# Optimization experiments

Measured on AMD Instinct MI355X. Metric: run time of the kernel, lower is better.

Reference implementation:

```python
import jax, jax.numpy as jnp
import numpy as np

SEQ, D_IN, D_OUT = 8192, 1024, 1024


def setup_inputs() -> dict:
    key = jax.random.key(0)
    kx, kq, kk, kv = jax.random.split(key, 4)
    # torch nn.Linear weights have shape (out_features, in_features)
    s = 1.0 / np.sqrt(D_IN)
    return {
        "x": jax.random.normal(kx, (SEQ, D_IN), dtype=jnp.float32),
        "Wq": jax.random.uniform(kq, (D_OUT, D_IN), dtype=jnp.float32, minval=-s, maxval=s),
        "Wk": jax.random.uniform(kk, (D_OUT, D_IN), dtype=jnp.float32, minval=-s, maxval=s),
        "Wv": jax.random.uniform(kv, (D_OUT, D_IN), dtype=jnp.float32, minval=-s, maxval=s),
    }


def reference(x, Wq, Wk, Wv):
    # Linear (no bias): y = x @ W.T
    q = x @ Wq.T          # [S, D_OUT]
    k = x @ Wk.T          # [S, D_OUT]
    v = x @ Wv.T          # [S, D_OUT]
    scale = 1.0 / jnp.sqrt(jnp.asarray(k.shape[-1], dtype=x.dtype))
    scores = (q @ k.T) * scale            # [S, S]
    weights = jax.nn.softmax(scores, axis=-1)
    return weights @ v                    # [S, D_OUT]
```

## Files before the change

kernel.cpp:

```cpp
#include <hip/hip_runtime.h>
#include <hip/hip_bf16.h>
#include <stdint.h>


#define SEQ 8192
#define DMODEL 1024
#define LOG2E 1.44269504088896340736f
#define GROUP_M 8

typedef __bf16 bf16_t;
typedef __bf16 bf16x8 __attribute__((ext_vector_type(8)));
typedef float f32x4 __attribute__((ext_vector_type(4)));

__global__ __launch_bounds__(256)
void convert_f32_bf16(const float* __restrict__ in, bf16_t* __restrict__ out, long n) {
    long i = ((long)blockIdx.x * 256 + threadIdx.x) * 4;
    if (i + 3 < n) {
        const float4 v = *(const float4*)(in + i);
        union { ushort4 u; bf16_t b[4]; } p;
        p.b[0] = (bf16_t)v.x; p.b[1] = (bf16_t)v.y;
        p.b[2] = (bf16_t)v.z; p.b[3] = (bf16_t)v.w;
        *(ushort4*)(out + i) = p.u;
    }
}

__global__ __launch_bounds__(256)
void add_f32(float* __restrict__ out, const float* __restrict__ part, long n) {
    long i = ((long)blockIdx.x * 256 + threadIdx.x) * 4;
    if (i + 3 < n) {
        float4 a = *(const float4*)(out + i);
        const float4 b = *(const float4*)(part + i);
        a.x += b.x; a.y += b.y; a.z += b.z; a.w += b.w;
        *(float4*)(out + i) = a;
    }
}

__global__ __launch_bounds__(256)
void zero_f32(float* __restrict__ p, int n) {
    int i = blockIdx.x * 256 + threadIdx.x;
    if (i < n) p[i] = 0.0f;
}

template <typename OutT, int MODE>
__global__ __launch_bounds__(512, 2)
void gemm_nt(const bf16_t* __restrict__ A, const bf16_t* __restrict__ B,
             OutT* __restrict__ C0, OutT* __restrict__ C1,
             float* __restrict__ lsum,
             int M, int N, int Kps, int lda, int ldb, int ldc,
             long plane, int cshift, float alpha)
{
    __shared__ bf16_t As[2][256 * 64];
    __shared__ bf16_t Bs[2][256 * 64];

    const int tid  = threadIdx.x;
    const int wave = tid >> 6;
    const int lane = tid & 63;

    const int nbm = M >> 8, nbn = N >> 8;
    const int tiles = nbm * nbn;
    int bid = blockIdx.x;
    const int sid = bid / tiles;
    bid -= sid * tiles;
    const long kbase = (long)sid * Kps;
    OutT* __restrict__ C = sid ? C1 : C0;

    const int per_group = GROUP_M * nbn;
    const int gid   = bid / per_group;
    const int rem   = bid - gid * per_group;
    const int first = gid * GROUP_M;
    const int gsz   = min(nbm - first, GROUP_M);
    const int bm    = first + rem % gsz;
    const int bn    = rem / gsz;
    const long row0 = (long)bm * 256;
    const long col0 = (long)bn * 256;

    const int wm = (wave >> 2) * 128;
    const int wn = (wave & 3) * 64;
    const int lr = lane & 15;
    const int lq = lane >> 4;

    const int rt = tid >> 3;
    const int sl = ((tid & 7) + rt) & 7;
    const bf16_t* pa = A + (row0 + rt) * (long)lda + kbase + sl * 8;
    const bf16_t* pb = B + (col0 + rt) * (long)ldb + kbase + sl * 8;

    const int p0  = (lq - lr) & 7;
    const int p1  = p0 ^ 4;
    const int oA0 = (wm + lr) * 64 + p0 * 8;
    const int oA1 = (wm + lr) * 64 + p1 * 8;
    const int oB0 = (wn + lr) * 64 + p0 * 8;
    const int oB1 = (wn + lr) * 64 + p1 * 8;

    const int nt = Kps >> 6;

    f32x4 acc[8][4] = {};

#define STG8(kt, bsel)                                                          \
    {                                                                           \
        _Pragma("unroll")                                                       \
        for (int i = 0; i < 4; ++i) {                                           \
            const bf16_t* ga = pa + (long)(kt) * 64 + (long)i * 64 * lda;       \
            __builtin_amdgcn_global_load_lds(                                   \
                (const __attribute__((address_space(1))) uint32_t*)ga,          \
                (__attribute__((address_space(3))) uint32_t*)(As[bsel] + i * 4096 + tid * 8), \
                16, 0, 0);                                                      \
        }                                                                       \
        _Pragma("unroll")                                                       \
        for (int i = 0; i < 4; ++i) {                                           \
            const bf16_t* gb = pb + (long)(kt) * 64 + (long)i * 64 * ldb;       \
            __builtin_amdgcn_global_load_lds(                                   \
                (const __attribute__((address_space(1))) uint32_t*)gb,          \
                (__attribute__((address_space(3))) uint32_t*)(Bs[bsel] + i * 4096 + tid * 8), \
                16, 0, 0);                                                      \
        }                                                                       \
    }

    STG8(0, 0);

    for (int t = 0; t < nt; ++t) {
        const int c = t & 1;
        const bf16_t* as = As[c];
        const bf16_t* bs = Bs[c];

        asm volatile("s_waitcnt vmcnt(0)" ::: "memory");
        __builtin_amdgcn_s_barrier();
        asm volatile("" ::: "memory");

        if (t + 1 < nt) STG8(t + 1, c ^ 1);

        bf16x8 a0k0[4], a0k1[4], b0k0[2], b0k1[2], b1k0[2], b1k1[2];
        #pragma unroll
        for (int mi = 0; mi < 4; ++mi) {
            a0k0[mi] = *(const bf16x8*)(as + oA0 + mi * 1024);
            a0k1[mi] = *(const bf16x8*)(as + oA1 + mi * 1024);
        }
        #pragma unroll
        for (int ni = 0; ni < 2; ++ni) {
            b0k0[ni] = *(const bf16x8*)(bs + oB0 + ni * 1024);
            b0k1[ni] = *(const bf16x8*)(bs + oB1 + ni * 1024);
            b1k0[ni] = *(const bf16x8*)(bs + oB0 + (ni + 2) * 1024);
            b1k1[ni] = *(const bf16x8*)(bs + oB1 + (ni + 2) * 1024);
        }

        __builtin_amdgcn_s_setprio(1);
        #pragma unroll
        for (int mi = 0; mi < 4; ++mi)
            #pragma unroll
            for (int ni = 0; ni < 2; ++ni)
                acc[mi][ni] = __builtin_amdgcn_mfma_f32_16x16x32_bf16(
                    a0k0[mi], b0k0[ni], acc[mi][ni], 0, 0, 0);
        #pragma unroll
        for (int mi = 0; mi < 4; ++mi)
            #pragma unroll
            for (int ni = 0; ni < 2; ++ni)
                acc[mi][ni] = __builtin_amdgcn_mfma_f32_16x16x32_bf16(
                    a0k1[mi], b0k1[ni], acc[mi][ni], 0, 0, 0);

        #pragma unroll
        for (int mi = 0; mi < 4; ++mi)
            #pragma unroll
            for (int ni = 0; ni < 2; ++ni)
                acc[mi][ni + 2] = __builtin_amdgcn_mfma_f32_16x16x32_bf16(
                    a0k0[mi], b1k0[ni], acc[mi][ni + 2], 0, 0, 0);
        #pragma unroll
        for (int mi = 0; mi < 4; ++mi)
            #pragma unroll
            for (int ni = 0; ni < 2; ++ni)
                acc[mi][ni + 2] = __builtin_amdgcn_mfma_f32_16x16x32_bf16(
                    a0k1[mi], b1k1[ni], acc[mi][ni + 2], 0, 0, 0);
        __builtin_amdgcn_s_setprio(0);

        bf16x8 a1k0[4], a1k1[4];
        #pragma unroll
        for (int mi = 0; mi < 4; ++mi) {
            a1k0[mi] = *(const bf16x8*)(as + oA0 + (mi + 4) * 1024);
            a1k1[mi] = *(const bf16x8*)(as + oA1 + (mi + 4) * 1024);
        }

        __builtin_amdgcn_s_setprio(1);
        #pragma unroll
        for (int mi = 0; mi < 4; ++mi)
            #pragma unroll
            for (int ni = 0; ni < 2; ++ni)
                acc[mi + 4][ni] = __builtin_amdgcn_mfma_f32_16x16x32_bf16(
                    a1k0[mi], b0k0[ni], acc[mi + 4][ni], 0, 0, 0);
        #pragma unroll
        for (int mi = 0; mi < 4; ++mi)
            #pragma unroll
            for (int ni = 0; ni < 2; ++ni)
                acc[mi + 4][ni] = __builtin_amdgcn_mfma_f32_16x16x32_bf16(
                    a1k1[mi], b0k1[ni], acc[mi + 4][ni], 0, 0, 0);

        #pragma unroll
        for (int mi = 0; mi < 4; ++mi)
            #pragma unroll
            for (int ni = 0; ni < 2; ++ni)
                acc[mi + 4][ni + 2] = __builtin_amdgcn_mfma_f32_16x16x32_bf16(
                    a1k0[mi], b1k0[ni], acc[mi + 4][ni + 2], 0, 0, 0);
        #pragma unroll
        for (int mi = 0; mi < 4; ++mi)
            #pragma unroll
            for (int ni = 0; ni < 2; ++ni)
                acc[mi + 4][ni + 2] = __builtin_amdgcn_mfma_f32_16x16x32_bf16(
                    a1k1[mi], b1k1[ni], acc[mi + 4][ni + 2], 0, 0, 0);
        __builtin_amdgcn_s_setprio(0);
    }
#undef STG8

    OutT* __restrict__ Cb = C + (col0 >> cshift) * plane;
    const int ccol0 = (int)(col0 & (((long)1 << cshift) - 1));

    if (MODE == 1) {
        #pragma unroll
        for (int mi = 0; mi < 8; ++mi)
            #pragma unroll
            for (int rg = 0; rg < 4; ++rg) {
                const long r = row0 + wm + mi * 16 + lq * 4 + rg;
                float part = 0.f;
                #pragma unroll
                for (int ni = 0; ni < 4; ++ni) {
                    const int cc = ccol0 + wn + ni * 16 + lr;
                    const float e = exp2f(alpha * acc[mi][ni][rg]);
                    part += e;
                    Cb[r * (long)ldc + cc] = (OutT)e;
                }
                part += __shfl_xor(part, 1);
                part += __shfl_xor(part, 2);
                part += __shfl_xor(part, 4);
                part += __shfl_xor(part, 8);
                if (lr == 0) atomicAdd(&lsum[r], part);
            }
    } else if (MODE == 2) {
        #pragma unroll
        for (int mi = 0; mi < 8; ++mi)
            #pragma unroll
            for (int rg = 0; rg < 4; ++rg) {
                const long r = row0 + wm + mi * 16 + lq * 4 + rg;
                const float inv = 1.0f / lsum[r];
                #pragma unroll
                for (int ni = 0; ni < 4; ++ni) {
                    const int cc = ccol0 + wn + ni * 16 + lr;
                    Cb[r * (long)ldc + cc] = (OutT)(acc[mi][ni][rg] * inv);
                }
            }
    } else {
        #pragma unroll
        for (int mi = 0; mi < 8; ++mi)
            #pragma unroll
            for (int ni = 0; ni < 4; ++ni)
                #pragma unroll
                for (int rg = 0; rg < 4; ++rg) {
                    const long r = row0 + wm + mi * 16 + lq * 4 + rg;
                    const int  cc = ccol0 + wn + ni * 16 + lr;
                    Cb[r * (long)ldc + cc] = (OutT)(alpha * acc[mi][ni][rg]);
                }
    }
}

__global__ __launch_bounds__(256)
void transpose_bf16(const bf16_t* __restrict__ in, bf16_t* __restrict__ out,
                    int R, int ldin, int ldout)
{
    __shared__ bf16_t tile[32][33];
    const int tx = threadIdx.x & 31;
    const int ty = threadIdx.x >> 5;
    const int c0 = blockIdx.x * 32;
    const int r0 = blockIdx.y * 32;
    #pragma unroll
    for (int j = 0; j < 32; j += 8)
        tile[ty + j][tx] = in[(long)(r0 + ty + j) * ldin + c0 + tx];
    __syncthreads();
    #pragma unroll
    for (int j = 0; j < 32; j += 8)
        out[(long)(c0 + ty + j) * ldout + r0 + tx] = tile[tx][ty + j];
}

extern "C" void kernel_launch(void* const* d_in, const int* in_sizes, int n_in,
                              void* d_out, int out_size, void* d_ws, size_t ws_size,
                              hipStream_t stream)
{
    const float* x  = (const float*)d_in[0];
    const float* Wq = (const float*)d_in[1];
    const float* Wk = (const float*)d_in[2];
    const float* Wv = (const float*)d_in[3];
    float* out = (float*)d_out;

    char* ws = (char*)d_ws;
    const long XN = (long)SEQ * DMODEL;
    const long WN = (long)DMODEL * DMODEL;
    const long SN = (long)SEQ * SEQ;

    bf16_t* xb   = (bf16_t*)ws;
    bf16_t* wcat = (bf16_t*)(ws + XN * 2);
    bf16_t* qb   = (bf16_t*)(ws + XN * 2 + WN * 6);
    bf16_t* kb   = qb + XN;
    bf16_t* vb   = qb + 2 * XN;
    bf16_t* Sb   = (bf16_t*)(ws + XN * 2 + WN * 6 + XN * 6);
    float*  pvp  = (float*)(ws + XN * 2 + WN * 6 + XN * 6 + SN * 2);
    float*  lsum = (float*)(ws + XN * 2 + WN * 6 + XN * 6 + SN * 2 + XN * 4);
    bf16_t* vtb  = xb;

    const size_t base_need = (size_t)(XN * 2 + WN * 6 + XN * 6 + SN * 2);
    const bool use_split = ws_size >= base_need + XN * 4 + SEQ * 4;
    if (!use_split) lsum = (float*)(ws + base_need);

    convert_f32_bf16<<<(int)(XN / 4 / 256), 256, 0, stream>>>(x,  xb, XN);
    convert_f32_bf16<<<(int)(WN / 4 / 256), 256, 0, stream>>>(Wq, wcat,          WN);
    convert_f32_bf16<<<(int)(WN / 4 / 256), 256, 0, stream>>>(Wk, wcat + WN,     WN);
    convert_f32_bf16<<<(int)(WN / 4 / 256), 256, 0, stream>>>(Wv, wcat + 2 * WN, WN);
    zero_f32<<<SEQ / 256, 256, 0, stream>>>(lsum, SEQ);

    dim3 blk256(256);
    dim3 blk512(512);
    gemm_nt<bf16_t, 0><<<(SEQ / 256) * (3 * DMODEL / 256), blk512, 0, stream>>>(
        xb, wcat, qb, qb, nullptr, SEQ, 3 * DMODEL, DMODEL,
        DMODEL, DMODEL, DMODEL, XN, 10, 1.0f);

    transpose_bf16<<<dim3(DMODEL / 32, SEQ / 32), blk256, 0, stream>>>(
        vb, vtb, SEQ, DMODEL, SEQ);

    gemm_nt<bf16_t, 1><<<(SEQ / 256) * (SEQ / 256), blk512, 0, stream>>>(
        qb, kb, Sb, Sb, lsum, SEQ, SEQ, DMODEL,
        DMODEL, DMODEL, SEQ, 0, 30, 0.03125f * LOG2E);

    if (use_split) {
        gemm_nt<float, 2><<<2 * (SEQ / 256) * (DMODEL / 256), blk512, 0, stream>>>(
            Sb, vtb, out, pvp, lsum, SEQ, DMODEL, SEQ / 2,
            SEQ, SEQ, DMODEL, 0, 30, 1.0f);
        add_f32<<<(int)(XN / 4 / 256), 256, 0, stream>>>(out, pvp, XN);
    } else {
        gemm_nt<float, 2><<<(SEQ / 256) * (DMODEL / 256), blk512, 0, stream>>>(
            Sb, vtb, out, out, lsum, SEQ, DMODEL, SEQ,
            SEQ, SEQ, DMODEL, 0, 30, 1.0f);
    }
}
```

Measured before the change: 512.0 us.

## Load B operand directly from global into registers for QKV and QK^T GEMMs

Adds a BDIR template path in which each wave loads its B fragments straight from global memory into registers, double-buffered across k-steps, while only A is staged through LDS. This halves LDS use for those GEMMs (which may allow more blocks per CU) and removes LDS reads for B. The cost is redundant global/L2 traffic, because waves sharing columns each fetch B separately, and higher register pressure. The PV GEMM keeps the original LDS path for both operands.

```diff
diff --git a/kernel.cpp b/kernel.cpp
--- a/kernel.cpp
+++ b/kernel.cpp
@@ -41,7 +41,7 @@
     if (i < n) p[i] = 0.0f;
 }
 
-template <typename OutT, int MODE>
+template <typename OutT, int MODE, int BDIR>
 __global__ __launch_bounds__(512, 2)
 void gemm_nt(const bf16_t* __restrict__ A, const bf16_t* __restrict__ B,
              OutT* __restrict__ C0, OutT* __restrict__ C1,
@@ -49,8 +49,7 @@
              int M, int N, int Kps, int lda, int ldb, int ldc,
              long plane, int cshift, float alpha)
 {
-    __shared__ bf16_t As[2][256 * 64];
-    __shared__ bf16_t Bs[2][256 * 64];
+    __shared__ bf16_t smem[(BDIR ? 2 : 4) * 16384];
 
     const int tid  = threadIdx.x;
     const int wave = tid >> 6;
@@ -95,117 +94,196 @@
 
     f32x4 acc[8][4] = {};
 
-#define STG8(kt, bsel)                                                          \
+#define STG4(kt, base, psrc, ld)                                                \
     {                                                                           \
         _Pragma("unroll")                                                       \
         for (int i = 0; i < 4; ++i) {                                           \
-            const bf16_t* ga = pa + (long)(kt) * 64 + (long)i * 64 * lda;       \
+            const bf16_t* g_ = (psrc) + (long)(kt) * 64 + (long)i * 64 * (ld);  \
             __builtin_amdgcn_global_load_lds(                                   \
-                (const __attribute__((address_space(1))) uint32_t*)ga,          \
-                (__attribute__((address_space(3))) uint32_t*)(As[bsel] + i * 4096 + tid * 8), \
+                (const __attribute__((address_space(1))) uint32_t*)g_,          \
+                (__attribute__((address_space(3))) uint32_t*)((base) + i * 4096 + tid * 8), \
                 16, 0, 0);                                                      \
         }                                                                       \
-        _Pragma("unroll")                                                       \
-        for (int i = 0; i < 4; ++i) {                                           \
-            const bf16_t* gb = pb + (long)(kt) * 64 + (long)i * 64 * ldb;       \
-            __builtin_amdgcn_global_load_lds(                                   \
-                (const __attribute__((address_space(1))) uint32_t*)gb,          \
-                (__attribute__((address_space(3))) uint32_t*)(Bs[bsel] + i * 4096 + tid * 8), \
-                16, 0, 0);                                                      \
-        }                                                                       \
-    }
-
-    STG8(0, 0);
-
-    for (int t = 0; t < nt; ++t) {
-        const int c = t & 1;
-        const bf16_t* as = As[c];
-        const bf16_t* bs = Bs[c];
-
-        asm volatile("s_waitcnt vmcnt(0)" ::: "memory");
-        __builtin_amdgcn_s_barrier();
-        asm volatile("" ::: "memory");
-
-        if (t + 1 < nt) STG8(t + 1, c ^ 1);
-
-        bf16x8 a0k0[4], a0k1[4], b0k0[2], b0k1[2], b1k0[2], b1k1[2];
-        #pragma unroll
-        for (int mi = 0; mi < 4; ++mi) {
-            a0k0[mi] = *(const bf16x8*)(as + oA0 + mi * 1024);
-            a0k1[mi] = *(const bf16x8*)(as + oA1 + mi * 1024);
+    }
+
+    if constexpr (BDIR) {
+        const bf16_t* gB[4];
+        #pragma unroll
+        for (int ni = 0; ni < 4; ++ni)
+            gB[ni] = B + (col0 + wn + ni * 16 + lr) * (long)ldb + kbase + lq * 8;
+
+        bf16x8 bA[8], bB[8];
+
+        #pragma unroll
+        for (int ni = 0; ni < 4; ++ni) {
+            bA[ni * 2 + 0] = *(const bf16x8*)(gB[ni]);
+            bA[ni * 2 + 1] = *(const bf16x8*)(gB[ni] + 32);
         }
-        #pragma unroll
-        for (int ni = 0; ni < 2; ++ni) {
-            b0k0[ni] = *(const bf16x8*)(bs + oB0 + ni * 1024);
-            b0k1[ni] = *(const bf16x8*)(bs + oB1 + ni * 1024);
-            b1k0[ni] = *(const bf16x8*)(bs + oB0 + (ni + 2) * 1024);
-            b1k1[ni] = *(const bf16x8*)(bs + oB1 + (ni + 2) * 1024);
+        STG4(0, smem, pa, lda);
+        #pragma unroll
+        for (int ni = 0; ni < 4; ++ni) gB[ni] += 64;
+
+#define BDIR_BODY(t, BU, BF)                                                    \
+        {                                                                       \
+            const int c_ = (t) & 1;                                             \
+            const bf16_t* as = smem + c_ * 16384;                               \
+                        \
+            asm volatile("s_waitcnt vmcnt(0)" ::: "memory");                    \
+            __builtin_amdgcn_s_barrier();                                       \
+            asm volatile("" ::: "memory");                                      \
+            if ((t) + 1 < nt) {                                                 \
+                _Pragma("unroll")                                               \
+                for (int ni = 0; ni < 4; ++ni) {                                \
+                    BF[ni * 2 + 0] = *(const bf16x8*)(gB[ni]);                  \
+                    BF[ni * 2 + 1] = *(const bf16x8*)(gB[ni] + 32);             \
+                }                                                               \
+                STG4((t) + 1, smem + (c_ ^ 1) * 16384, pa, lda);                \
+            }                                                                   \
+            _Pragma("unroll")                                                   \
+            for (int ni = 0; ni < 4; ++ni) gB[ni] += 64;                        \
+            bf16x8 a0[4], a1[4];                                                \
+            _Pragma("unroll")                                                   \
+            for (int mi = 0; mi < 4; ++mi) {                                    \
+                a0[mi] = *(const bf16x8*)(as + oA0 + mi * 1024);                \
+                a1[mi] = *(const bf16x8*)(as + oA1 + mi * 1024);                \
+            }                                                                   \
+            __builtin_amdgcn_s_setprio(1);                                      \
+            _Pragma("unroll")                                                   \
+            for (int mi = 0; mi < 4; ++mi)                                      \
+                _Pragma("unroll")                                               \
+                for (int ni = 0; ni < 4; ++ni)                                  \
+                    acc[mi][ni] = __builtin_amdgcn_mfma_f32_16x16x32_bf16(      \
+                        a0[mi], BU[ni * 2 + 0], acc[mi][ni], 0, 0, 0);          \
+            _Pragma("unroll")                                                   \
+            for (int mi = 0; mi < 4; ++mi)                                      \
+                _Pragma("unroll")                                               \
+                for (int ni = 0; ni < 4; ++ni)                                  \
+                    acc[mi][ni] = __builtin_amdgcn_mfma_f32_16x16x32_bf16(      \
+                        a1[mi], BU[ni * 2 + 1], acc[mi][ni], 0, 0, 0);          \
+            __builtin_amdgcn_s_setprio(0);                                      \
+            bf16x8 a2[4], a3[4];                                                \
+            _Pragma("unroll")                                                   \
+            for (int mi = 0; mi < 4; ++mi) {                                    \
+                a2[mi] = *(const bf16x8*)(as + oA0 + (mi + 4) * 1024);          \
+                a3[mi] = *(const bf16x8*)(as + oA1 + (mi + 4) * 1024);          \
+            }                                                                   \
+            __builtin_amdgcn_s_setprio(1);                                      \
+            _Pragma("unroll")                                                   \
+            for (int mi = 0; mi < 4; ++mi)                                      \
+                _Pragma("unroll")                                               \
+                for (int ni = 0; ni < 4; ++ni)                                  \
+                    acc[mi + 4][ni] = __builtin_amdgcn_mfma_f32_16x16x32_bf16(  \
+                        a2[mi], BU[ni * 2 + 0], acc[mi + 4][ni], 0, 0, 0);      \
+            _Pragma("unroll")                                                   \
+            for (int mi = 0; mi < 4; ++mi)                                      \
+                _Pragma("unroll")                                               \
+                for (int ni = 0; ni < 4; ++ni)                                  \
+                    acc[mi + 4][ni] = __builtin_amdgcn_mfma_f32_16x16x32_bf16(  \
+                        a3[mi], BU[ni * 2 + 1], acc[mi + 4][ni], 0, 0, 0);      \
+            __builtin_amdgcn_s_setprio(0);                                      \
         }
 
-        __builtin_amdgcn_s_setprio(1);
-        #pragma unroll
-        for (int mi = 0; mi < 4; ++mi)
-            #pragma unroll
-            for (int ni = 0; ni < 2; ++ni)
-                acc[mi][ni] = __builtin_amdgcn_mfma_f32_16x16x32_bf16(
-                    a0k0[mi], b0k0[ni], acc[mi][ni], 0, 0, 0);
-        #pragma unroll
-        for (int mi = 0; mi < 4; ++mi)
-            #pragma unroll
-            for (int ni = 0; ni < 2; ++ni)
-                acc[mi][ni] = __builtin_amdgcn_mfma_f32_16x16x32_bf16(
-                    a0k1[mi], b0k1[ni], acc[mi][ni], 0, 0, 0);
-
-        #pragma unroll
-        for (int mi = 0; mi < 4; ++mi)
-            #pragma unroll
-            for (int ni = 0; ni < 2; ++ni)
-                acc[mi][ni + 2] = __builtin_amdgcn_mfma_f32_16x16x32_bf16(
-                    a0k0[mi], b1k0[ni], acc[mi][ni + 2], 0, 0, 0);
-        #pragma unroll
-        for (int mi = 0; mi < 4; ++mi)
-            #pragma unroll
-            for (int ni = 0; ni < 2; ++ni)
-                acc[mi][ni + 2] = __builtin_amdgcn_mfma_f32_16x16x32_bf16(
-                    a0k1[mi], b1k1[ni], acc[mi][ni + 2], 0, 0, 0);
-        __builtin_amdgcn_s_setprio(0);
-
-        bf16x8 a1k0[4], a1k1[4];
-        #pragma unroll
-        for (int mi = 0; mi < 4; ++mi) {
-            a1k0[mi] = *(const bf16x8*)(as + oA0 + (mi + 4) * 1024);
-            a1k1[mi] = *(const bf16x8*)(as + oA1 + (mi + 4) * 1024);
+        for (int t = 0; t < nt; t += 2) {
+            BDIR_BODY(t,     bA, bB);
+            BDIR_BODY(t + 1, bB, bA);
         }
-
-        __builtin_amdgcn_s_setprio(1);
-        #pragma unroll
-        for (int mi = 0; mi < 4; ++mi)
-            #pragma unroll
-            for (int ni = 0; ni < 2; ++ni)
-                acc[mi + 4][ni] = __builtin_amdgcn_mfma_f32_16x16x32_bf16(
-                    a1k0[mi], b0k0[ni], acc[mi + 4][ni], 0, 0, 0);
-        #pragma unroll
-        for (int mi = 0; mi < 4; ++mi)
-            #pragma unroll
-            for (int ni = 0; ni < 2; ++ni)
-                acc[mi + 4][ni] = __builtin_amdgcn_mfma_f32_16x16x32_bf16(
-                    a1k1[mi], b0k1[ni], acc[mi + 4][ni], 0, 0, 0);
-
-        #pragma unroll
-        for (int mi = 0; mi < 4; ++mi)
-            #pragma unroll
-            for (int ni = 0; ni < 2; ++ni)
-                acc[mi + 4][ni + 2] = __builtin_amdgcn_mfma_f32_16x16x32_bf16(
-                    a1k0[mi], b1k0[ni], acc[mi + 4][ni + 2], 0, 0, 0);
-        #pragma unroll
-        for (int mi = 0; mi < 4; ++mi)
-            #pragma unroll
-            for (int ni = 0; ni < 2; ++ni)
-                acc[mi + 4][ni + 2] = __builtin_amdgcn_mfma_f32_16x16x32_bf16(
-                    a1k1[mi], b1k1[ni], acc[mi + 4][ni + 2], 0, 0, 0);
-        __builtin_amdgcn_s_setprio(0);
-    }
-#undef STG8
+#undef BDIR_BODY
+    } else {
+        bf16_t* const Bbase = smem + 2 * 16384;
+        STG4(0, smem, pa, lda);
+        STG4(0, Bbase, pb, ldb);
+
+        for (int t = 0; t < nt; ++t) {
+            const int c = t & 1;
+            const bf16_t* as = smem  + c * 16384;
+            const bf16_t* bs = Bbase + c * 16384;
+
+            asm volatile("s_waitcnt vmcnt(0)" ::: "memory");
+            __builtin_amdgcn_s_barrier();
+            asm volatile("" ::: "memory");
+
+            if (t + 1 < nt) {
+                STG4(t + 1, smem  + (c ^ 1) * 16384, pa, lda);
+                STG4(t + 1, Bbase + (c ^ 1) * 16384, pb, ldb);
+            }
+
+            bf16x8 a0k0[4], a0k1[4], b0k0[2], b0k1[2], b1k0[2], b1k1[2];
+            #pragma unroll
+            for (int mi = 0; mi < 4; ++mi) {
+                a0k0[mi] = *(const bf16x8*)(as + oA0 + mi * 1024);
+                a0k1[mi] = *(const bf16x8*)(as + oA1 + mi * 1024);
+            }
+            #pragma unroll
+            for (int ni = 0; ni < 2; ++ni) {
+                b0k0[ni] = *(const bf16x8*)(bs + oB0 + ni * 1024);
+                b0k1[ni] = *(const bf16x8*)(bs + oB1 + ni * 1024);
+                b1k0[ni] = *(const bf16x8*)(bs + oB0 + (ni + 2) * 1024);
+                b1k1[ni] = *(const bf16x8*)(bs + oB1 + (ni + 2) * 1024);
+            }
+
+            __builtin_amdgcn_s_setprio(1);
+            #pragma unroll
+            for (int mi = 0; mi < 4; ++mi)
+                #pragma unroll
+                for (int ni = 0; ni < 2; ++ni)
+                    acc[mi][ni] = __builtin_amdgcn_mfma_f32_16x16x32_bf16(
+                        a0k0[mi], b0k0[ni], acc[mi][ni], 0, 0, 0);
+            #pragma unroll
+            for (int mi = 0; mi < 4; ++mi)
+                #pragma unroll
+                for (int ni = 0; ni < 2; ++ni)
+                    acc[mi][ni] = __builtin_amdgcn_mfma_f32_16x16x32_bf16(
+                        a0k1[mi], b0k1[ni], acc[mi][ni], 0, 0, 0);
+            #pragma unroll
+            for (int mi = 0; mi < 4; ++mi)
+                #pragma unroll
+                for (int ni = 0; ni < 2; ++ni)
+                    acc[mi][ni + 2] = __builtin_amdgcn_mfma_f32_16x16x32_bf16(
+                        a0k0[mi], b1k0[ni], acc[mi][ni + 2], 0, 0, 0);
+            #pragma unroll
+            for (int mi = 0; mi < 4; ++mi)
+                #pragma unroll
+                for (int ni = 0; ni < 2; ++ni)
+                    acc[mi][ni + 2] = __builtin_amdgcn_mfma_f32_16x16x32_bf16(
+                        a0k1[mi], b1k1[ni], acc[mi][ni + 2], 0, 0, 0);
+            __builtin_amdgcn_s_setprio(0);
+
+            bf16x8 a1k0[4], a1k1[4];
+            #pragma unroll
+            for (int mi = 0; mi < 4; ++mi) {
+                a1k0[mi] = *(const bf16x8*)(as + oA0 + (mi + 4) * 1024);
+                a1k1[mi] = *(const bf16x8*)(as + oA1 + (mi + 4) * 1024);
+            }
+
+            __builtin_amdgcn_s_setprio(1);
+            #pragma unroll
+            for (int mi = 0; mi < 4; ++mi)
+                #pragma unroll
+                for (int ni = 0; ni < 2; ++ni)
+                    acc[mi + 4][ni] = __builtin_amdgcn_mfma_f32_16x16x32_bf16(
+                        a1k0[mi], b0k0[ni], acc[mi + 4][ni], 0, 0, 0);
+            #pragma unroll
+            for (int mi = 0; mi < 4; ++mi)
+                #pragma unroll
+                for (int ni = 0; ni < 2; ++ni)
+                    acc[mi + 4][ni] = __builtin_amdgcn_mfma_f32_16x16x32_bf16(
+                        a1k1[mi], b0k1[ni], acc[mi + 4][ni], 0, 0, 0);
+            #pragma unroll
+            for (int mi = 0; mi < 4; ++mi)
+                #pragma unroll
+                for (int ni = 0; ni < 2; ++ni)
+                    acc[mi + 4][ni + 2] = __builtin_amdgcn_mfma_f32_16x16x32_bf16(
+                        a1k0[mi], b1k0[ni], acc[mi + 4][ni + 2], 0, 0, 0);
+            #pragma unroll
+            for (int mi = 0; mi < 4; ++mi)
+                #pragma unroll
+                for (int ni = 0; ni < 2; ++ni)
+                    acc[mi + 4][ni + 2] = __builtin_amdgcn_mfma_f32_16x16x32_bf16(
+                        a1k1[mi], b1k1[ni], acc[mi + 4][ni + 2], 0, 0, 0);
+            __builtin_amdgcn_s_setprio(0);
+        }
+    }
+#undef STG4
 
     OutT* __restrict__ Cb = C + (col0 >> cshift) * plane;
     const int ccol0 = (int)(col0 & (((long)1 << cshift) - 1));
@@ -312,24 +390,24 @@
 
     dim3 blk256(256);
     dim3 blk512(512);
-    gemm_nt<bf16_t, 0><<<(SEQ / 256) * (3 * DMODEL / 256), blk512, 0, stream>>>(
+    gemm_nt<bf16_t, 0, 1><<<(SEQ / 256) * (3 * DMODEL / 256), blk512, 0, stream>>>(
         xb, wcat, qb, qb, nullptr, SEQ, 3 * DMODEL, DMODEL,
         DMODEL, DMODEL, DMODEL, XN, 10, 1.0f);
 
     transpose_bf16<<<dim3(DMODEL / 32, SEQ / 32), blk256, 0, stream>>>(
         vb, vtb, SEQ, DMODEL, SEQ);
 
-    gemm_nt<bf16_t, 1><<<(SEQ / 256) * (SEQ / 256), blk512, 0, stream>>>(
+    gemm_nt<bf16_t, 1, 1><<<(SEQ / 256) * (SEQ / 256), blk512, 0, stream>>>(
         qb, kb, Sb, Sb, lsum, SEQ, SEQ, DMODEL,
         DMODEL, DMODEL, SEQ, 0, 30, 0.03125f * LOG2E);
 
     if (use_split) {
-        gemm_nt<float, 2><<<2 * (SEQ / 256) * (DMODEL / 256), blk512, 0, stream>>>(
+        gemm_nt<float, 2, 0><<<2 * (SEQ / 256) * (DMODEL / 256), blk512, 0, stream>>>(
             Sb, vtb, out, pvp, lsum, SEQ, DMODEL, SEQ / 2,
             SEQ, SEQ, DMODEL, 0, 30, 1.0f);
         add_f32<<<(int)(XN / 4 / 256), 256, 0, stream>>>(out, pvp, XN);
     } else {
-        gemm_nt<float, 2><<<(SEQ / 256) * (DMODEL / 256), blk512, 0, stream>>>(
+        gemm_nt<float, 2, 0><<<(SEQ / 256) * (DMODEL / 256), blk512, 0, stream>>>(
             Sb, vtb, out, out, lsum, SEQ, DMODEL, SEQ,
             SEQ, SEQ, DMODEL, 0, 30, 1.0f);
     }
```

Result: slower. 648.7 us (+26.7%).
